# Kernel tuning notes

Measured on AMD Instinct MI355X. Metric: run time of the kernel, lower is better.

The kernel has to match this reference:

```python
import jax, jax.numpy as jnp
import numpy as np

E = 1024   # embd_size
H = 16     # heads_num
DH = E // H
DFF = 4 * E
B, T = 2, 2048


def layer_norm(x, g, b, eps=1e-5):
    mu = jnp.mean(x, axis=-1, keepdims=True)
    var = jnp.var(x, axis=-1, keepdims=True)
    return (x - mu) * jax.lax.rsqrt(var + eps) * g + b


def setup_inputs() -> dict:
    key = jax.random.key(0)
    ks = jax.random.split(key, 12)
    s = 0.02
    return {
        "x": jax.random.normal(ks[0], (B, T, E), dtype=jnp.float32),
        "Wq": jax.random.normal(ks[1], (E, E), dtype=jnp.float32) * s,
        "Wk": jax.random.normal(ks[2], (E, E), dtype=jnp.float32) * s,
        "Wv": jax.random.normal(ks[3], (E, E), dtype=jnp.float32) * s,
        "Wo": jax.random.normal(ks[4], (E, E), dtype=jnp.float32) * s,
        "bo": jnp.zeros((E,), dtype=jnp.float32),
        "W1": jax.random.normal(ks[5], (E, DFF), dtype=jnp.float32) * s,
        "b1": jnp.zeros((DFF,), dtype=jnp.float32),
        "W2": jax.random.normal(ks[6], (DFF, E), dtype=jnp.float32) * s,
        "b2": jnp.zeros((E,), dtype=jnp.float32),
        "g1": jnp.ones((E,), dtype=jnp.float32),
        "be1": jnp.zeros((E,), dtype=jnp.float32),
        "g2": jnp.ones((E,), dtype=jnp.float32),
        "be2": jnp.zeros((E,), dtype=jnp.float32),
    }


def reference(x, Wq, Wk, Wv, Wo, bo, W1, b1, W2, b2, g1, be1, g2, be2):
    Bx, Tx, C = x.shape
    # --- self-attention sublayer ---
    h = layer_norm(x, g1, be1)
    # per-head projections; heads concatenated along output dim == stacked weights
    q = (h @ Wq).reshape(Bx, Tx, H, DH)  # [B,T,H,Dh]
    k = (h @ Wk).reshape(Bx, Tx, H, DH)
    v = (h @ Wv).reshape(Bx, Tx, H, DH)
    # NOTE: original scales by full embd_size**-0.5 (C = x.shape[-1]), not head_size
    scale = C ** (-0.5)
    scores = jnp.einsum("bqhd,bkhd->bhqk", q, k) * scale  # [B,H,T,T]
    mask = jnp.tril(jnp.ones((Tx, Tx), dtype=bool))
    scores = jnp.where(mask, scores, -jnp.inf)
    attn = jax.nn.softmax(scores, axis=-1)
    o = jnp.einsum("bhqk,bkhd->bqhd", attn, v).reshape(Bx, Tx, C)
    sa = o @ Wo + bo
    x = x + sa
    # --- feed-forward sublayer ---
    h2 = layer_norm(x, g2, be2)
    ff = jax.nn.relu(h2 @ W1 + b1) @ W2 + b2
    return x + ff
```

## Files before the change

### kernel.cpp

```cpp
#include <hip/hip_runtime.h>
#include <hip/hip_bf16.h>
#include <math.h>

#define Bn 2
#define Tn 2048
#define En 1024
#define Hn 16
#define DFFn 4096
#define Mn (Bn*Tn)
#define QKVLD 3072

typedef __hip_bfloat16 bf16;
typedef unsigned short u16;
typedef unsigned int u32;
typedef __attribute__((ext_vector_type(8))) short short8;
typedef __attribute__((ext_vector_type(4))) float f32x4;

typedef __attribute__((address_space(1))) const void cg_void;
typedef __attribute__((address_space(3))) void lds_void;

#define QSC 0.0450842200278f

#define HBAR() asm volatile("s_waitcnt lgkmcnt(0)\n\ts_barrier" ::: "memory")

__device__ __forceinline__ u16 f2bf(float f) {
    bf16 h = __float2bfloat16(f);
    u16 u; __builtin_memcpy(&u, &h, 2); return u;
}
__device__ __forceinline__ float bf2f(u16 u) {
    u32 x = ((u32)u) << 16; float f; __builtin_memcpy(&f, &x, 4); return f;
}

__global__ __launch_bounds__(256)
void transpose_w4(const float* __restrict__ s0, const float* __restrict__ s1,
                  const float* __restrict__ s2, const float* __restrict__ s3,
                  u16* __restrict__ d0, u16* __restrict__ d1,
                  u16* __restrict__ d2, u16* __restrict__ d3) {
    const float* src = (blockIdx.z == 0) ? s0 : (blockIdx.z == 1) ? s1
                     : (blockIdx.z == 2) ? s2 : s3;
    u16* dst = (blockIdx.z == 0) ? d0 : (blockIdx.z == 1) ? d1
             : (blockIdx.z == 2) ? d2 : d3;
    __shared__ float t[64][65];
    const int r0 = blockIdx.y * 64, c0 = blockIdx.x * 64;
    const int tr = threadIdx.x >> 6, tc = threadIdx.x & 63;
#pragma unroll
    for (int i = 0; i < 16; i++)
        t[tr + i * 4][tc] = src[(size_t)(r0 + tr + i * 4) * 1024 + c0 + tc];
    __syncthreads();
#pragma unroll
    for (int i = 0; i < 16; i++)
        dst[(size_t)(c0 + tr + i * 4) * 1024 + r0 + tc] = f2bf(t[tc][tr + i * 4]);
}

__global__ __launch_bounds__(256)
void transpose_w(const float* __restrict__ src, u16* __restrict__ dst,
                 int R, int C) {
    __shared__ float t[64][65];
    const int r0 = blockIdx.y * 64, c0 = blockIdx.x * 64;
    const int tr = threadIdx.x >> 6, tc = threadIdx.x & 63;
#pragma unroll
    for (int i = 0; i < 16; i++)
        t[tr + i * 4][tc] = src[(size_t)(r0 + tr + i * 4) * C + c0 + tc];
    __syncthreads();
#pragma unroll
    for (int i = 0; i < 16; i++)
        dst[(size_t)(c0 + tr + i * 4) * R + r0 + tc] = f2bf(t[tc][tr + i * 4]);
}

__global__ __launch_bounds__(256)
void vcopy_t(const u16* __restrict__ QKV, u16* __restrict__ Vg) {
    const int bh = blockIdx.z;
    const int t0 = blockIdx.y * 64;
    __shared__ u16 t[64][65];
    const int tr = threadIdx.x >> 6, tc = threadIdx.x & 63;
    const u16* src = QKV + (size_t)(bh >> 4) * 2048 * QKVLD + 2048 + (bh & 15) * 64;
#pragma unroll
    for (int i = 0; i < 16; i++)
        t[tr + i * 4][tc] = src[(size_t)(t0 + tr + i * 4) * QKVLD + tc];
    __syncthreads();
    u16* dst = Vg + (size_t)bh * 64 * 2048;
#pragma unroll
    for (int i = 0; i < 16; i++)
        dst[(size_t)(tr + i * 4) * 2048 + t0 + tc] = t[tc][tr + i * 4];
}

template<typename AT>
__global__ __launch_bounds__(256)
void ln_kernel(const AT* __restrict__ x, const float* __restrict__ g,
               const float* __restrict__ b, u16* __restrict__ out) {
    const int row = blockIdx.x;
    const int tid = threadIdx.x;
    const AT* xp = x + (size_t)row * En;
    float v[4];
    float s = 0.f, sq = 0.f;
#pragma unroll
    for (int i = 0; i < 4; i++) {
        if constexpr (sizeof(AT) == 2) v[i] = bf2f(xp[tid + i * 256]);
        else                           v[i] = (float)xp[tid + i * 256];
        s += v[i];
        sq += v[i] * v[i];
    }
    __shared__ float rs[256], rq[256];
    rs[tid] = s; rq[tid] = sq;
    __syncthreads();
    for (int st = 128; st > 0; st >>= 1) {
        if (tid < st) { rs[tid] += rs[tid + st]; rq[tid] += rq[tid + st]; }
        __syncthreads();
    }
    const float mu  = rs[0] * (1.0f / En);
    const float var = rq[0] * (1.0f / En) - mu * mu;
    const float inv = rsqrtf(var + 1e-5f);
#pragma unroll
    for (int i = 0; i < 4; i++) {
        const int c = tid + i * 256;
        out[(size_t)row * En + c] = f2bf((v[i] - mu) * inv * g[c] + b[c]);
    }
}

template<int TM, int HAS_BIAS, int RELU, int RES, int OUT_F32, int SCQ,
         int SPLITC, int SPLITA>
__global__ __launch_bounds__(256)
void gemm_bt(const u16* __restrict__ A, const u16* __restrict__ A2, int ldA,
             const u16* __restrict__ Wt, int ldW,
             const float* __restrict__ bias, const void* __restrict__ res,
             void* __restrict__ Cout, void* __restrict__ Cout2,
             int ldC, int Kd) {
    constexpr int IF = TM / 32;
    __shared__ __align__(16) u16 As[TM * 32];
    __shared__ __align__(16) u16 Bs[128 * 32];
    const int tid  = threadIdx.x;
    const int lane = tid & 63, wv = tid >> 6;
    const int quad = lane >> 4, l16 = lane & 15;
    const int m0 = blockIdx.y * TM, n0 = blockIdx.x * 128;
    const int rw = (wv >> 1) * (TM / 2), cw = (wv & 1) * 64;
    const int lr  = lane >> 2;
    const int gsw = ((lane & 3) ^ ((lane >> 3) & 3)) * 8;
    const int psw = (quad ^ ((l16 >> 1) & 3)) * 8;

    f32x4 acc[IF][4] = {};

    for (int kt = 0; kt < Kd; kt += 32) {
        const u16* Ap = (SPLITA && kt >= 2048) ? A2 : A;
        const int  kk = SPLITA ? (kt & 2047) : kt;
        __syncthreads();
#pragma unroll
        for (int t = 0; t < TM / 64; t++) {
            const int row = wv * (TM / 4) + t * 16;
            __builtin_amdgcn_global_load_lds(
                (cg_void*)(const void*)&Ap[(size_t)(m0 + row + lr) * ldA + kk + gsw],
                (lds_void*)(void*)&As[row * 32], 16, 0, 0);
        }
#pragma unroll
        for (int t = 0; t < 2; t++) {
            const int row = wv * 32 + t * 16;
            __builtin_amdgcn_global_load_lds(
                (cg_void*)(const void*)&Wt[(size_t)(n0 + row + lr) * ldW + kt + gsw],
                (lds_void*)(void*)&Bs[row * 32], 16, 0, 0);
        }
        __syncthreads();

        short8 af[IF], bfr[4];
#pragma unroll
        for (int i = 0; i < IF; i++)
            af[i] = *(const short8*)&As[(rw + i * 16 + l16) * 32 + psw];
#pragma unroll
        for (int j = 0; j < 4; j++)
            bfr[j] = *(const short8*)&Bs[(cw + j * 16 + l16) * 32 + psw];
#pragma unroll
        for (int i = 0; i < IF; i++)
#pragma unroll
            for (int j = 0; j < 4; j++)
                acc[i][j] = __builtin_amdgcn_mfma_f32_16x16x32_bf16(
                    af[i], bfr[j], acc[i][j], 0, 0, 0);
    }

    const float qscale = (SCQ && n0 < 1024) ? QSC : 1.0f;
    void* Cp = (SPLITC && n0 >= 2048) ? Cout2 : Cout;
#pragma unroll
    for (int i = 0; i < IF; i++) {
#pragma unroll
        for (int r = 0; r < 4; r++) {
            const int gm = m0 + rw + i * 16 + quad * 4 + r;
#pragma unroll
            for (int j = 0; j < 4; j++) {
                const int gn = n0 + cw + j * 16 + l16;
                const int cn = SPLITC ? (gn & 2047) : gn;
                float c = acc[i][j][r];
                if (HAS_BIAS) c += bias[gn];
                if (RELU) c = fmaxf(c, 0.f);
                if (RES == 1) c += ((const float*)res)[(size_t)gm * ldC + cn];
                if (RES == 2) c += bf2f(((const u16*)res)[(size_t)gm * ldC + cn]);
                if (SCQ) c *= qscale;
                if (OUT_F32) ((float*)Cp)[(size_t)gm * ldC + cn] = c;
                else         ((u16*)Cp)[(size_t)gm * ldC + cn] = f2bf(c);
            }
        }
    }
}

__global__ __launch_bounds__(256)
void flash_pass1(const u16* __restrict__ QKV, const u16* __restrict__ Vg,
                 u16* __restrict__ Op0, u16* __restrict__ Op1qkv,
                 float* __restrict__ stats) {
    const int pr = blockIdx.x >> 1, half = blockIdx.x & 1;
    const int hh = blockIdx.y, bb = blockIdx.z;
    const int tid  = threadIdx.x;
    const int lane = tid & 63, wv = tid >> 6;
    const int quad = lane >> 4, l16 = lane & 15;

    __shared__ __align__(16) u16 Ks[2][64 * 64];
    __shared__ __align__(16) u16 Vt[2][64 * 64];
    __shared__ __align__(16) u16 Ps[4][16 * 64];

    const size_t rowbase = (size_t)(bb * Tn) * QKVLD;
    const u16* Vgh = Vg + (size_t)(bb * Hn + hh) * 64 * 2048;

    const int sr = tid >> 2;
    const int p0 = (tid & 3) | ((sr & 1) << 2);
    const int p1 = p0 ^ 4;
    const int g0 = p0 ^ (sr & 7), g1 = p1 ^ (sr & 7);
    const int lsw = l16 & 7;

    uint4 kA, kB, vA, vB;
    auto prefetch = [&](int kt) {
        const size_t kb = rowbase + (size_t)(kt * 64 + sr) * QKVLD + 1024 + hh * 64;
        kA = *(const uint4*)&QKV[kb + g0 * 8];
        kB = *(const uint4*)&QKV[kb + g1 * 8];
        const size_t vb = (size_t)sr * 2048 + kt * 64;
        vA = *(const uint4*)&Vgh[vb + g0 * 8];
        vB = *(const uint4*)&Vgh[vb + g1 * 8];
    };
    auto writebuf = [&](int buf) {
        *(uint4*)&Ks[buf][sr * 64 + p0 * 8] = kA;
        *(uint4*)&Ks[buf][sr * 64 + p1 * 8] = kB;
        *(uint4*)&Vt[buf][sr * 64 + p0 * 8] = vA;
        *(uint4*)&Vt[buf][sr * 64 + p1 * 8] = vB;
    };

    for (int qsel = 0; qsel < 2; qsel++) {
        const int qt = qsel ? (31 - pr) : pr;
        const int nk = (qt >= half) ? ((qt - half) >> 1) + 1 : 0;
        const int qrow = qt * 64 + wv * 16 + l16;
        const int grow = bb * Tn + qrow;

        f32x4 ot[4] = {};
        float m2 = -INFINITY, lrow = 0.f;

        HBAR();
        if (nk > 0) {
            const u16* qp = QKV + rowbase + (size_t)qrow * QKVLD + hh * 64;
            short8 qf[2];
            qf[0] = *(const short8*)&qp[quad * 8];
            qf[1] = *(const short8*)&qp[32 + quad * 8];

            prefetch(half);
            writebuf(0);
            if (nk > 1) prefetch(half + 2);
            HBAR();

            const bool hasdiag = ((qt ^ half) & 1) == 0;
            for (int f = 0; f < nk; f++) {
                const int cur = f & 1;

                f32x4 st[4] = {};
#pragma unroll
                for (int ks = 0; ks < 2; ks++)
#pragma unroll
                    for (int i = 0; i < 4; i++) {
                        short8 kf = *(const short8*)&Ks[cur][(i * 16 + l16) * 64 +
                                     (((ks * 4 + quad) ^ lsw) * 8)];
                        st[i] = __builtin_amdgcn_mfma_f32_16x16x32_bf16(
                            kf, qf[ks], st[i], 0, 0, 0);
                    }

                float tmax = -INFINITY;
                if (hasdiag && f == nk - 1) {
                    const int qloc = wv * 16 + l16;
#pragma unroll
                    for (int i = 0; i < 4; i++)
#pragma unroll
                        for (int r = 0; r < 4; r++) {
                            float s = st[i][r];
                            if (i * 16 + quad * 4 + r > qloc) s = -INFINITY;
                            st[i][r] = s;
                            tmax = fmaxf(tmax, s);
                        }
                } else {
#pragma unroll
                    for (int i = 0; i < 4; i++)
#pragma unroll
                        for (int r = 0; r < 4; r++)
                            tmax = fmaxf(tmax, st[i][r]);
                }
                tmax = fmaxf(tmax, __shfl_xor(tmax, 16));
                tmax = fmaxf(tmax, __shfl_xor(tmax, 32));

                const float mnew = fmaxf(m2, tmax);
                const float alpha = exp2f(m2 - mnew);
                m2 = mnew;
                float psum = 0.f;
#pragma unroll
                for (int i = 0; i < 4; i++)
#pragma unroll
                    for (int r = 0; r < 4; r++) {
                        const float e = exp2f(st[i][r] - mnew);
                        st[i][r] = e;
                        psum += e;
                    }
                psum += __shfl_xor(psum, 16);
                psum += __shfl_xor(psum, 32);
                lrow = lrow * alpha + psum;
#pragma unroll
                for (int i = 0; i < 4; i++) ot[i] *= alpha;

#pragma unroll
                for (int i = 0; i < 4; i++) {
                    uint2 w;
                    w.x = (u32)f2bf(st[i][0]) | ((u32)f2bf(st[i][1]) << 16);
                    w.y = (u32)f2bf(st[i][2]) | ((u32)f2bf(st[i][3]) << 16);
                    const int g = (i * 2 + (quad >> 1)) ^ lsw;
                    *(uint2*)&Ps[wv][l16 * 64 + g * 8 + (quad & 1) * 4] = w;
                }
                asm volatile("s_waitcnt lgkmcnt(0)" ::: "memory");

#pragma unroll
                for (int ks = 0; ks < 2; ks++) {
                    short8 pf = *(const short8*)&Ps[wv][l16 * 64 +
                                 (((ks * 4 + quad) ^ lsw) * 8)];
#pragma unroll
                    for (int i = 0; i < 4; i++) {
                        short8 vf = *(const short8*)&Vt[cur][(i * 16 + l16) * 64 +
                                     (((ks * 4 + quad) ^ lsw) * 8)];
                        ot[i] = __builtin_amdgcn_mfma_f32_16x16x32_bf16(
                            vf, pf, ot[i], 0, 0, 0);
                    }
                }

                if (f + 1 < nk) {
                    writebuf(cur ^ 1);
                    if (f + 2 < nk) prefetch(half + 2 * (f + 2));
                    HBAR();
                }
            }
        }

        u16* op = (half == 0) ? (Op0 + (size_t)grow * 1024 + hh * 64)
                              : (Op1qkv + (size_t)grow * QKVLD + 2048 + hh * 64);
#pragma unroll
        for (int i = 0; i < 4; i++) {
            ushort4 o4;
            o4.x = f2bf(ot[i][0]); o4.y = f2bf(ot[i][1]);
            o4.z = f2bf(ot[i][2]); o4.w = f2bf(ot[i][3]);
            *(ushort4*)&op[i * 16 + quad * 4] = o4;
        }
        if (quad == 0) {
            stats[((size_t)(half * 2 + 0) * 4096 + grow) * 16 + hh] = m2;
            stats[((size_t)(half * 2 + 1) * 4096 + grow) * 16 + hh] = lrow;
        }
    }
}

__global__ __launch_bounds__(256)
void flash_merge(u16* __restrict__ QKV, const u16* __restrict__ Op0,
                 const float* __restrict__ stats) {
    const int row = blockIdx.x;
    const int tid = threadIdx.x;
    const int col = tid * 4;
    const int hh = col >> 6;
    const float m0 = stats[((size_t)0 * 4096 + row) * 16 + hh];
    const float l0 = stats[((size_t)1 * 4096 + row) * 16 + hh];
    const float m1 = stats[((size_t)2 * 4096 + row) * 16 + hh];
    const float l1 = stats[((size_t)3 * 4096 + row) * 16 + hh];
    const float m  = fmaxf(m0, m1);
    const float w0 = exp2f(m0 - m), w1 = exp2f(m1 - m);
    const float inv = 1.0f / (w0 * l0 + w1 * l1);
    ushort4 a = *(const ushort4*)&Op0[(size_t)row * 1024 + col];
    ushort4 b = *(const ushort4*)&QKV[(size_t)row * QKVLD + 2048 + col];
    ushort4 o;
    o.x = f2bf((w0 * bf2f(a.x) + w1 * bf2f(b.x)) * inv);
    o.y = f2bf((w0 * bf2f(a.y) + w1 * bf2f(b.y)) * inv);
    o.z = f2bf((w0 * bf2f(a.z) + w1 * bf2f(b.z)) * inv);
    o.w = f2bf((w0 * bf2f(a.w) + w1 * bf2f(b.w)) * inv);
    *(ushort4*)&QKV[(size_t)row * QKVLD + col] = o;
}

extern "C" void kernel_launch(void* const* d_in, const int* in_sizes, int n_in,
                              void* d_out, int out_size, void* d_ws, size_t ws_size,
                              hipStream_t stream) {
    const float* x   = (const float*)d_in[0];
    const float* Wq  = (const float*)d_in[1];
    const float* Wk  = (const float*)d_in[2];
    const float* Wv  = (const float*)d_in[3];
    const float* Wo  = (const float*)d_in[4];
    const float* bo  = (const float*)d_in[5];
    const float* W1  = (const float*)d_in[6];
    const float* b1  = (const float*)d_in[7];
    const float* W2  = (const float*)d_in[8];
    const float* b2  = (const float*)d_in[9];
    const float* g1  = (const float*)d_in[10];
    const float* be1 = (const float*)d_in[11];
    const float* g2  = (const float*)d_in[12];
    const float* be2 = (const float*)d_in[13];

    char* wsb = (char*)d_ws;
    u16*   QKV = (u16*)wsb;
    u16*   F1a = (u16*)wsb;
    u16*   W2T = (u16*)(wsb + 16u * 1024 * 1024);
    u16*   Op0 = (u16*)(wsb + 24u * 1024 * 1024);
    u16*   X1b = Op0;
    u16*   Vg  = (u16*)(wsb + 32u * 1024 * 1024);
    u16*   F1b = Vg;
    u16*   h     = (u16*)d_out;
    u16*   WT    = (u16*)((char*)d_out + 8u * 1024 * 1024);
    u16*   WqkvT = WT;
    u16*   WoT   = WT + 3u * 1024 * 1024;
    float* stats = (float*)WT;
    u16*   W1T   = WT;

    transpose_w4<<<dim3(16, 16, 4), 256, 0, stream>>>(
        Wq, Wk, Wv, Wo,
        WqkvT, WqkvT + 1024u * 1024, WqkvT + 2048u * 1024, WoT);

    ln_kernel<float><<<Mn, 256, 0, stream>>>(x, g1, be1, h);

    gemm_bt<128, 0, 0, 0, 0, 1, 0, 0><<<dim3(24, 32), 256, 0, stream>>>(
        h, nullptr, En, WqkvT, En, nullptr, nullptr, QKV, nullptr, QKVLD, En);

    vcopy_t<<<dim3(1, 32, 32), 256, 0, stream>>>(QKV, Vg);

    flash_pass1<<<dim3(32, Hn, Bn), 256, 0, stream>>>(QKV, Vg, Op0, QKV, stats);

    flash_merge<<<Mn, 256, 0, stream>>>(QKV, Op0, stats);

    gemm_bt<64, 1, 0, 1, 0, 0, 0, 0><<<dim3(8, 64), 256, 0, stream>>>(
        QKV, nullptr, QKVLD, WoT, En, bo, x, X1b, nullptr, En, En);

    transpose_w<<<dim3(64, 16), 256, 0, stream>>>(W1, W1T, 1024, 4096);
    transpose_w<<<dim3(16, 64), 256, 0, stream>>>(W2, W2T, 4096, 1024);

    ln_kernel<u16><<<Mn, 256, 0, stream>>>(X1b, g2, be2, h);

    gemm_bt<128, 1, 1, 0, 0, 0, 1, 0><<<dim3(32, 32), 256, 0, stream>>>(
        h, nullptr, En, W1T, En, b1, nullptr, F1a, F1b, 2048, En);

    gemm_bt<64, 1, 0, 2, 1, 0, 0, 1><<<dim3(8, 64), 256, 0, stream>>>(
        F1a, F1b, 2048, W2T, DFFn, b2, X1b, (float*)d_out, nullptr, En, DFFn);
}
```

Measured before the change: 386.9 us.

## Split-K the FF2 GEMM across two blocks with atomic accumulation

The second feed-forward GEMM (K=4096) is split along K into two halves via a grid z dimension, each accumulating into the fp32 output with atomicAdd. A new init kernel first writes residual plus bias into the output so the GEMM epilogue only adds partial sums. This doubles the block count of a 512-block launch to improve CU occupancy, at the cost of an extra init pass and atomic traffic on the output.

New measurement: 400.8 us. +3.6%, slower.

```diff
diff --git a/kernel.cpp b/kernel.cpp
--- a/kernel.cpp
+++ b/kernel.cpp
@@ -117,8 +117,23 @@
     }
 }
 
+__global__ __launch_bounds__(256)
+void ff2_init(const u16* __restrict__ X1, const float* __restrict__ b2,
+              float* __restrict__ out) {
+    const int row = blockIdx.x;
+    const int c = threadIdx.x * 4;
+    ushort4 a = *(const ushort4*)&X1[(size_t)row * En + c];
+    float4 bb = *(const float4*)&b2[c];
+    float4 o;
+    o.x = bf2f(a.x) + bb.x;
+    o.y = bf2f(a.y) + bb.y;
+    o.z = bf2f(a.z) + bb.z;
+    o.w = bf2f(a.w) + bb.w;
+    *(float4*)&out[(size_t)row * En + c] = o;
+}
+
 template<int TM, int HAS_BIAS, int RELU, int RES, int OUT_F32, int SCQ,
-         int SPLITC, int SPLITA>
+         int SPLITC, int SPLITA, int ATOM = 0>
 __global__ __launch_bounds__(256)
 void gemm_bt(const u16* __restrict__ A, const u16* __restrict__ A2, int ldA,
              const u16* __restrict__ Wt, int ldW,
@@ -139,7 +154,8 @@
 
     f32x4 acc[IF][4] = {};
 
-    for (int kt = 0; kt < Kd; kt += 32) {
+    const int kbase = ATOM ? (int)blockIdx.z * Kd : 0;
+    for (int kt = kbase; kt < kbase + Kd; kt += 32) {
         const u16* Ap = (SPLITA && kt >= 2048) ? A2 : A;
         const int  kk = SPLITA ? (kt & 2047) : kt;
         __syncthreads();
@@ -191,8 +207,13 @@
                 if (RES == 1) c += ((const float*)res)[(size_t)gm * ldC + cn];
                 if (RES == 2) c += bf2f(((const u16*)res)[(size_t)gm * ldC + cn]);
                 if (SCQ) c *= qscale;
-                if (OUT_F32) ((float*)Cp)[(size_t)gm * ldC + cn] = c;
-                else         ((u16*)Cp)[(size_t)gm * ldC + cn] = f2bf(c);
+                if (ATOM) {
+                    atomicAdd(&((float*)Cp)[(size_t)gm * ldC + cn], c);
+                } else if (OUT_F32) {
+                    ((float*)Cp)[(size_t)gm * ldC + cn] = c;
+                } else {
+                    ((u16*)Cp)[(size_t)gm * ldC + cn] = f2bf(c);
+                }
             }
         }
     }
@@ -443,6 +464,9 @@
     gemm_bt<128, 1, 1, 0, 0, 0, 1, 0><<<dim3(32, 32), 256, 0, stream>>>(
         h, nullptr, En, W1T, En, b1, nullptr, F1a, F1b, 2048, En);
 
-    gemm_bt<64, 1, 0, 2, 1, 0, 0, 1><<<dim3(8, 64), 256, 0, stream>>>(
-        F1a, F1b, 2048, W2T, DFFn, b2, X1b, (float*)d_out, nullptr, En, DFFn);
-}
+    ff2_init<<<Mn, 256, 0, stream>>>(X1b, b2, (float*)d_out);
+
+    gemm_bt<64, 0, 0, 0, 1, 0, 0, 1, 1><<<dim3(8, 64, 2), 256, 0, stream>>>(
+        F1a, F1b, 2048, W2T, DFFn, nullptr, nullptr, (float*)d_out, nullptr,
+        En, 2048);
+}
```
